# Performance work log

Measured on AMD Instinct MI355X. Metric: run time of the kernel, lower is better.

The kernel has to match this reference:

```python
import jax, jax.numpy as jnp
import numpy as np


def setup_inputs() -> dict:
    key = jax.random.key(0)
    k1, k2, k3, k4, k5 = jax.random.split(key, 5)
    B, N, E, C_in, C_out, K = 64, 4096, 16, 64, 64, 3
    return {
        "x": jax.random.normal(k1, (B, N, C_in), dtype=jnp.float32),
        "adj_matrix": jax.random.normal(k2, (N, E), dtype=jnp.float32),
        "adj_embeddings": jax.random.normal(k3, (E, N), dtype=jnp.float32),
        "weights": jax.random.normal(k4, (K, C_in, C_out), dtype=jnp.float32) * 0.1,
        "bias": jax.random.normal(k5, (C_out,), dtype=jnp.float32) * 0.1,
    }


def reference(x, adj_matrix, adj_embeddings, weights, bias):
    # x: [B, N, C_in]; adj_matrix: [N, E]; adj_embeddings: [E, N]
    N = adj_matrix.shape[0]
    cheb_k = weights.shape[0]
    # adaptive adjacency: softmax(relu(adj @ emb), axis=1) -> [N, N]
    supports = jax.nn.softmax(jax.nn.relu(adj_matrix @ adj_embeddings), axis=1)
    # Chebyshev polynomial recursion: T0 = I, T1 = supports,
    # Tk = 2*supports @ T_{k-1} - T_{k-2}
    support_set = [jnp.eye(N, dtype=supports.dtype), supports]
    for _ in range(2, cheb_k):
        support_set.append(2.0 * supports @ support_set[-1] - support_set[-2])
    supports_k = jnp.stack(support_set, axis=0)  # [K, N, N]
    # aggregate: [K,N,M] x [B,M,C] -> [B,N,K,C]
    x_g = jnp.einsum("knm,bmc->bnkc", supports_k, x)
    # mix: [B,N,K,Cin] x [K,Cin,Cout] -> [B,N,Cout]
    return jnp.einsum("bnki,kio->bno", x_g, weights) + bias
```

## Files before the change

### kernel.cpp

```cpp
#include <hip/hip_runtime.h>


typedef __bf16 bf16;
typedef __bf16 bf16x8 __attribute__((ext_vector_type(8)));
typedef float f32x4 __attribute__((ext_vector_type(4)));

__device__ __forceinline__ void async_lds16(const void* g, void* l) {
  __builtin_amdgcn_global_load_lds((const __attribute__((address_space(1))) void*)g,
                                   (__attribute__((address_space(3))) void*)l, 16, 0, 0);
}

#define FENCE() asm volatile("" ::: "memory")
#define BAR()                          \
  do {                                 \
    FENCE();                           \
    __builtin_amdgcn_s_barrier();      \
    FENCE();                           \
  } while (0)
#define WAIT_VM(n) asm volatile("s_waitcnt vmcnt(" #n ")" ::: "memory")

__global__ __launch_bounds__(256) void build_wcat_k(const float* __restrict__ w, bf16* __restrict__ Wc) {
  int idx = blockIdx.x * 256 + threadIdx.x;
  if (idx >= 64 * 192) return;
  int o = idx / 192, kk = idx - o * 192;
  int k = kk >> 6, i = kk & 63;
  float v;
  if (k == 0)      v = w[i * 64 + o] - w[2 * 4096 + i * 64 + o];
  else if (k == 1) v = w[4096 + i * 64 + o];
  else             v = 2.f * w[2 * 4096 + i * 64 + o];
  Wc[idx] = (bf16)v;
}

__global__ __launch_bounds__(256) void supports_k(const float* __restrict__ adj,
                                                  const float* __restrict__ emb,
                                                  bf16* __restrict__ S) {
  __shared__ float sadj[8][16];
  __shared__ float sred[4];
  const int tid = threadIdx.x;
  const int n0 = blockIdx.x * 8;
  if (tid < 128) sadj[tid >> 4][tid & 15] = adj[n0 * 16 + tid];
  __syncthreads();
  for (int r = 0; r < 8; ++r) {
    float vals[16];
    float mx = 0.f;
    #pragma unroll
    for (int it = 0; it < 16; ++it) {
      const int j = it * 256 + tid;
      float v = 0.f;
      #pragma unroll
      for (int e = 0; e < 16; ++e) v = fmaf(sadj[r][e], emb[e * 4096 + j], v);
      v = fmaxf(v, 0.f);
      vals[it] = v;
      mx = fmaxf(mx, v);
    }
    #pragma unroll
    for (int off = 32; off > 0; off >>= 1) mx = fmaxf(mx, __shfl_xor(mx, off, 64));
    if ((tid & 63) == 0) sred[tid >> 6] = mx;
    __syncthreads();
    mx = fmaxf(fmaxf(sred[0], sred[1]), fmaxf(sred[2], sred[3]));
    float sum = 0.f;
    #pragma unroll
    for (int it = 0; it < 16; ++it) {
      float ev = __expf(vals[it] - mx);
      vals[it] = ev;
      sum += ev;
    }
    #pragma unroll
    for (int off = 32; off > 0; off >>= 1) sum += __shfl_xor(sum, off, 64);
    __syncthreads();
    if ((tid & 63) == 0) sred[tid >> 6] = sum;
    __syncthreads();
    const float inv = 1.f / (sred[0] + sred[1] + sred[2] + sred[3]);
    bf16* Srow = S + (n0 + r) * 4096;
    #pragma unroll
    for (int it = 0; it < 16; ++it) Srow[it * 256 + tid] = (bf16)(vals[it] * inv);
    __syncthreads();
  }
}

__global__ __launch_bounds__(256) void xpose_x_k(const float* __restrict__ x, bf16* __restrict__ Xt) {
  __shared__ float tile[64][65];
  const int tid = threadIdx.x;
  const int mt = blockIdx.x, b = blockIdx.y;
  const float* src = x + (b * 4096 + mt * 64) * 64;
  #pragma unroll
  for (int it = 0; it < 16; ++it) {
    const int idx = it * 256 + tid;
    tile[idx >> 6][idx & 63] = src[idx];
  }
  __syncthreads();
  #pragma unroll
  for (int it = 0; it < 16; ++it) {
    const int idx = it * 256 + tid;
    const int rr = idx >> 6, cc = idx & 63;
    Xt[(b * 64 + rr) * 4096 + mt * 64 + cc] = (bf16)tile[cc][rr];
  }
}

__global__ __launch_bounds__(256) void transpose_bf16_k(const bf16* __restrict__ in, bf16* __restrict__ outT) {
  __shared__ bf16 tile[64][65];
  const int tid = threadIdx.x;
  const int ti = blockIdx.x & 63, tj = blockIdx.x >> 6;
  #pragma unroll
  for (int it = 0; it < 16; ++it) {
    const int idx = it * 256 + tid;
    tile[idx >> 6][idx & 63] = in[(ti * 64 + (idx >> 6)) * 4096 + tj * 64 + (idx & 63)];
  }
  __syncthreads();
  #pragma unroll
  for (int it = 0; it < 16; ++it) {
    const int idx = it * 256 + tid;
    const int rr = idx >> 6, cc = idx & 63;
    outT[(tj * 64 + rr) * 4096 + ti * 64 + cc] = tile[cc][rr];
  }
}

__global__ __launch_bounds__(512, 2) void gemm256_k(const bf16* __restrict__ A,
                                                    const bf16* __restrict__ Bt,
                                                    bf16* __restrict__ C) {
  __shared__ bf16 As[2][2][256][32];
  __shared__ bf16 Bs[2][2][256][32];

  const int tid = threadIdx.x;
  const int bid = blockIdx.x;
  const int wg = (bid & 7) * 32 + (bid >> 3);
  const int tm = wg >> 4, tn = wg & 15;
  const int rowBase = tm * 256, colBase = tn * 256;

  const int wv = tid >> 6, lane = tid & 63;
  const int wm = wv >> 2, wn = wv & 3;
  const int t16 = lane & 15, quad = lane >> 4;
  const int wv16 = wv * 16;
  const int q8 = (quad ^ ((t16 >> 1) & 3)) * 8;
  const int wm128 = wm * 128;
  const int wn64 = wn * 64;

  const int sr = tid >> 2;
  const int sc = ((tid & 3) ^ ((tid >> 3) & 3)) * 8;
  const bf16* gA = A + (size_t)(rowBase + sr) * 4096 + sc;
  const bf16* gB = Bt + (size_t)(colBase + sr) * 4096 + sc;

  f32x4 acc[8][4];
  #pragma unroll
  for (int i = 0; i < 8; ++i)
    #pragma unroll
    for (int j = 0; j < 4; ++j) acc[i][j] = (f32x4){0.f, 0.f, 0.f, 0.f};

  auto stA = [&](int buf, int s, int k0) {
    async_lds16(gA + k0 + s * 32, &As[buf][s][wv16][0]);
    async_lds16(gA + 524288 + k0 + s * 32, &As[buf][s][128 + wv16][0]);
  };
  auto stB = [&](int buf, int s, int k0) {
    async_lds16(gB + k0 + s * 32, &Bs[buf][s][wv16][0]);
    async_lds16(gB + 524288 + k0 + s * 32, &Bs[buf][s][128 + wv16][0]);
  };

  bf16x8 Ra[4], Rb[4], B0[4], B1[4];
  auto rdA = [&](bf16x8* R, int buf, int s, int g) {
    #pragma unroll
    for (int i = 0; i < 4; ++i)
      R[i] = *(const bf16x8*)&As[buf][s][wm128 + (g * 4 + i) * 16 + t16][q8];
  };
  auto rdB = [&](bf16x8* R, int buf, int s) {
    #pragma unroll
    for (int j = 0; j < 4; ++j)
      R[j] = *(const bf16x8*)&Bs[buf][s][wn64 + j * 16 + t16][q8];
  };
  auto mfma16 = [&](int g, const bf16x8* R, const bf16x8* Bv) {
    __builtin_amdgcn_s_setprio(1);
    #pragma unroll
    for (int i = 0; i < 4; ++i)
      #pragma unroll
      for (int j = 0; j < 4; ++j)
        acc[g * 4 + i][j] =
            __builtin_amdgcn_mfma_f32_16x16x32_bf16(R[i], Bv[j], acc[g * 4 + i][j], 0, 0, 0);
    __builtin_amdgcn_s_setprio(0);
  };

  stB(0, 0, 0); stA(0, 0, 0); stB(0, 1, 0); stA(0, 1, 0);
  stB(1, 0, 64); stA(1, 0, 64); stB(1, 1, 64);
  WAIT_VM(6);
  BAR();
  rdA(Ra, 0, 0, 0);
  rdB(B0, 0, 0);

  for (int it = 0; it < 31; ++it) {
    const int kb = it * 128;
    rdA(Rb, 0, 0, 1); stA(1, 1, kb + 64);
    BAR(); mfma16(0, Ra, B0); BAR();
    rdA(Ra, 0, 1, 0); rdB(B1, 0, 1); stB(0, 0, kb + 128);
    BAR(); mfma16(1, Rb, B0); BAR();
    rdA(Rb, 0, 1, 1); stA(0, 0, kb + 128);
    BAR(); mfma16(0, Ra, B1); BAR();
    stB(0, 1, kb + 128); WAIT_VM(6);
    BAR();
    rdA(Ra, 1, 0, 0); rdB(B0, 1, 0);
    mfma16(1, Rb, B1); BAR();
    rdA(Rb, 1, 0, 1); stA(0, 1, kb + 128);
    BAR(); mfma16(0, Ra, B0); BAR();
    rdA(Ra, 1, 1, 0); rdB(B1, 1, 1); stB(1, 0, kb + 192);
    BAR(); mfma16(1, Rb, B0); BAR();
    rdA(Rb, 1, 1, 1); stA(1, 0, kb + 192);
    BAR(); mfma16(0, Ra, B1); BAR();
    stB(1, 1, kb + 192); WAIT_VM(6);
    BAR();
    rdA(Ra, 0, 0, 0); rdB(B0, 0, 0);
    mfma16(1, Rb, B1); BAR();
  }

  rdA(Rb, 0, 0, 1); stA(1, 1, 4032);
  BAR(); mfma16(0, Ra, B0); BAR();
  rdA(Ra, 0, 1, 0); rdB(B1, 0, 1);
  BAR(); mfma16(1, Rb, B0); BAR();
  rdA(Rb, 0, 1, 1);
  BAR(); mfma16(0, Ra, B1); BAR();
  WAIT_VM(0);
  BAR();
  rdA(Ra, 1, 0, 0); rdB(B0, 1, 0);
  mfma16(1, Rb, B1); BAR();
  rdA(Rb, 1, 0, 1);
  mfma16(0, Ra, B0);
  rdA(Ra, 1, 1, 0); rdB(B1, 1, 1);
  mfma16(1, Rb, B0);
  rdA(Rb, 1, 1, 1);
  mfma16(0, Ra, B1);
  mfma16(1, Rb, B1);

  #pragma unroll
  for (int i = 0; i < 8; ++i) {
    const int row0 = rowBase + wm128 + i * 16 + quad * 4;
    #pragma unroll
    for (int j = 0; j < 4; ++j) {
      const int col = colBase + wn64 + j * 16 + t16;
      #pragma unroll
      for (int rr = 0; rr < 4; ++rr)
        C[(size_t)(row0 + rr) * 4096 + col] = (bf16)acc[i][j][rr];
    }
  }
}

__global__ __launch_bounds__(256) void mix_k(const float* __restrict__ x, const bf16* __restrict__ XG1,
                                             const bf16* __restrict__ XG2, const bf16* __restrict__ Wc,
                                             const float* __restrict__ bias, float* __restrict__ out) {
  __shared__ bf16 sW[64 * 200];
  const int tid = threadIdx.x;
  const int nt = blockIdx.x, b = blockIdx.y;
  {
    const int rw = tid >> 2, part = tid & 3;
    #pragma unroll
    for (int v = 0; v < 6; ++v)
      *(bf16x8*)(sW + rw * 200 + part * 48 + v * 8) = *(const bf16x8*)(Wc + rw * 192 + part * 48 + v * 8);
  }
  __syncthreads();

  const int lane = tid & 63, wv = tid >> 6;
  const int t16 = lane & 15, quad = lane >> 4;
  const int nBase = nt * 128 + wv * 32;

  f32x4 acc[2][4];
  #pragma unroll
  for (int i = 0; i < 2; ++i)
    #pragma unroll
    for (int j = 0; j < 4; ++j) acc[i][j] = (f32x4){0.f, 0.f, 0.f, 0.f};

  #pragma unroll
  for (int ch = 0; ch < 6; ++ch) {
    bf16x8 a[2];
    #pragma unroll
    for (int i = 0; i < 2; ++i) {
      const int row = nBase + i * 16 + t16;
      if (ch < 2) {
        const float* p = x + (b * 4096 + row) * 64 + ch * 32 + quad * 8;
        float4 f0 = *(const float4*)p;
        float4 f1 = *(const float4*)(p + 4);
        bf16x8 t;
        t[0] = (bf16)f0.x; t[1] = (bf16)f0.y; t[2] = (bf16)f0.z; t[3] = (bf16)f0.w;
        t[4] = (bf16)f1.x; t[5] = (bf16)f1.y; t[6] = (bf16)f1.z; t[7] = (bf16)f1.w;
        a[i] = t;
      } else {
        const bf16* src = (ch < 4) ? XG1 : XG2;
        a[i] = *(const bf16x8*)(src + row * 4096 + b * 64 + (ch & 1) * 32 + quad * 8);
      }
    }
    #pragma unroll
    for (int j = 0; j < 4; ++j) {
      bf16x8 wf = *(const bf16x8*)(sW + (j * 16 + t16) * 200 + ch * 32 + quad * 8);
      #pragma unroll
      for (int i = 0; i < 2; ++i)
        acc[i][j] = __builtin_amdgcn_mfma_f32_16x16x32_bf16(a[i], wf, acc[i][j], 0, 0, 0);
    }
  }

  #pragma unroll
  for (int j = 0; j < 4; ++j) {
    const float bb = bias[j * 16 + t16];
    #pragma unroll
    for (int i = 0; i < 2; ++i) {
      const int n0 = nBase + i * 16 + quad * 4;
      #pragma unroll
      for (int rr = 0; rr < 4; ++rr)
        out[(b * 4096 + n0 + rr) * 64 + j * 16 + t16] = acc[i][j][rr] + bb;
    }
  }
}

extern "C" void kernel_launch(void* const* d_in, const int* in_sizes, int n_in,
                              void* d_out, int out_size, void* d_ws, size_t ws_size,
                              hipStream_t stream) {
  const float* x    = (const float*)d_in[0];
  const float* adj  = (const float*)d_in[1];
  const float* emb  = (const float*)d_in[2];
  const float* w    = (const float*)d_in[3];
  const float* bias = (const float*)d_in[4];
  float* out = (float*)d_out;

  char* ws = (char*)d_ws;
  const size_t SZ = (size_t)4096 * 4096 * sizeof(bf16);
  bf16* S    = (bf16*)(ws);
  bf16* XG1  = (bf16*)(ws + SZ);
  bf16* XG2  = (bf16*)(ws + 2 * SZ);
  bf16* XBUF = (bf16*)(ws + 3 * SZ);
  bf16* Wc   = (bf16*)(ws + 4 * SZ);

  build_wcat_k<<<48, 256, 0, stream>>>(w, Wc);
  supports_k<<<512, 256, 0, stream>>>(adj, emb, S);
  xpose_x_k<<<dim3(64, 64), 256, 0, stream>>>(x, XBUF);
  gemm256_k<<<256, 512, 0, stream>>>(S, XBUF, XG1);
  transpose_bf16_k<<<4096, 256, 0, stream>>>(XG1, XBUF);
  gemm256_k<<<256, 512, 0, stream>>>(S, XBUF, XG2);
  mix_k<<<dim3(32, 64), 256, 0, stream>>>(x, XG1, XG2, Wc, bias, out);
}
```

Baseline: 445.0 us.

## Restructure GEMM barrier schedule and fuse transposed store of first GEMM output

The GEMM main loop is reordered so each LDS read group is followed directly by its MFMA block with a single barrier per phase, where before every MFMA block was bracketed by two barriers. The aim is less barrier overhead and more overlap of LDS reads with matrix math. Separately, the first GEMM now also writes its output transposed into an extra workspace buffer, so the standalone transpose kernel is skipped when the workspace is large enough. This costs extra strided 8-byte global stores in the epilogue and one more buffer of workspace.

```diff
diff --git a/kernel.cpp b/kernel.cpp
--- a/kernel.cpp
+++ b/kernel.cpp
@@ -117,7 +117,8 @@
 
 __global__ __launch_bounds__(512, 2) void gemm256_k(const bf16* __restrict__ A,
                                                     const bf16* __restrict__ Bt,
-                                                    bf16* __restrict__ C) {
+                                                    bf16* __restrict__ C,
+                                                    bf16* __restrict__ Ct) {
   __shared__ bf16 As[2][2][256][32];
   __shared__ bf16 Bs[2][2][256][32];
 
@@ -181,44 +182,57 @@
   stB(1, 0, 64); stA(1, 0, 64); stB(1, 1, 64);
   WAIT_VM(6);
   BAR();
-  rdA(Ra, 0, 0, 0);
-  rdB(B0, 0, 0);
 
   for (int it = 0; it < 31; ++it) {
     const int kb = it * 128;
-    rdA(Rb, 0, 0, 1); stA(1, 1, kb + 64);
-    BAR(); mfma16(0, Ra, B0); BAR();
-    rdA(Ra, 0, 1, 0); rdB(B1, 0, 1); stB(0, 0, kb + 128);
-    BAR(); mfma16(1, Rb, B0); BAR();
-    rdA(Rb, 0, 1, 1); stA(0, 0, kb + 128);
-    BAR(); mfma16(0, Ra, B1); BAR();
-    stB(0, 1, kb + 128); WAIT_VM(6);
-    BAR();
-    rdA(Ra, 1, 0, 0); rdB(B0, 1, 0);
-    mfma16(1, Rb, B1); BAR();
-    rdA(Rb, 1, 0, 1); stA(0, 1, kb + 128);
-    BAR(); mfma16(0, Ra, B0); BAR();
-    rdA(Ra, 1, 1, 0); rdB(B1, 1, 1); stB(1, 0, kb + 192);
-    BAR(); mfma16(1, Rb, B0); BAR();
-    rdA(Rb, 1, 1, 1); stA(1, 0, kb + 192);
-    BAR(); mfma16(0, Ra, B1); BAR();
-    stB(1, 1, kb + 192); WAIT_VM(6);
-    BAR();
-    rdA(Ra, 0, 0, 0); rdB(B0, 0, 0);
-    mfma16(1, Rb, B1); BAR();
-  }
-
-  rdA(Rb, 0, 0, 1); stA(1, 1, 4032);
-  BAR(); mfma16(0, Ra, B0); BAR();
+    rdA(Ra, 0, 0, 0); rdB(B0, 0, 0); rdA(Rb, 0, 0, 1);
+    stA(1, 1, kb + 64);
+    mfma16(0, Ra, B0);
+    BAR();
+    rdA(Ra, 0, 1, 0); rdB(B1, 0, 1);
+    stB(0, 0, kb + 128);
+    mfma16(1, Rb, B0);
+    BAR();
+    rdA(Rb, 0, 1, 1);
+    stA(0, 0, kb + 128);
+    mfma16(0, Ra, B1);
+    BAR();
+    stB(0, 1, kb + 128);
+    mfma16(1, Rb, B1);
+    WAIT_VM(6);
+    BAR();
+    rdA(Ra, 1, 0, 0); rdB(B0, 1, 0); rdA(Rb, 1, 0, 1);
+    stA(0, 1, kb + 128);
+    mfma16(0, Ra, B0);
+    BAR();
+    rdA(Ra, 1, 1, 0); rdB(B1, 1, 1);
+    stB(1, 0, kb + 192);
+    mfma16(1, Rb, B0);
+    BAR();
+    rdA(Rb, 1, 1, 1);
+    stA(1, 0, kb + 192);
+    mfma16(0, Ra, B1);
+    BAR();
+    stB(1, 1, kb + 192);
+    mfma16(1, Rb, B1);
+    WAIT_VM(6);
+    BAR();
+  }
+
+  rdA(Ra, 0, 0, 0); rdB(B0, 0, 0); rdA(Rb, 0, 0, 1);
+  stA(1, 1, 4032);
+  mfma16(0, Ra, B0);
+  BAR();
   rdA(Ra, 0, 1, 0); rdB(B1, 0, 1);
-  BAR(); mfma16(1, Rb, B0); BAR();
+  mfma16(1, Rb, B0);
+  BAR();
   rdA(Rb, 0, 1, 1);
-  BAR(); mfma16(0, Ra, B1); BAR();
+  mfma16(0, Ra, B1);
+  BAR();
+  mfma16(1, Rb, B1);
   WAIT_VM(0);
   BAR();
-  rdA(Ra, 1, 0, 0); rdB(B0, 1, 0);
-  mfma16(1, Rb, B1); BAR();
-  rdA(Rb, 1, 0, 1);
+  rdA(Ra, 1, 0, 0); rdB(B0, 1, 0); rdA(Rb, 1, 0, 1);
   mfma16(0, Ra, B0);
   rdA(Ra, 1, 1, 0); rdB(B1, 1, 1);
   mfma16(1, Rb, B0);
@@ -235,6 +249,20 @@
       #pragma unroll
       for (int rr = 0; rr < 4; ++rr)
         C[(size_t)(row0 + rr) * 4096 + col] = (bf16)acc[i][j][rr];
+    }
+  }
+  if (Ct) {
+    #pragma unroll
+    for (int i = 0; i < 8; ++i) {
+      const int row0 = rowBase + wm128 + i * 16 + quad * 4;
+      #pragma unroll
+      for (int j = 0; j < 4; ++j) {
+        const int col = colBase + wn64 + j * 16 + t16;
+        union { bf16 h[4]; uint2 u; } pk;
+        #pragma unroll
+        for (int rr = 0; rr < 4; ++rr) pk.h[rr] = (bf16)acc[i][j][rr];
+        *(uint2*)(Ct + (size_t)col * 4096 + row0) = pk.u;
+      }
     }
   }
 }
@@ -320,13 +348,15 @@
   bf16* XG1  = (bf16*)(ws + SZ);
   bf16* XG2  = (bf16*)(ws + 2 * SZ);
   bf16* XBUF = (bf16*)(ws + 3 * SZ);
-  bf16* Wc   = (bf16*)(ws + 4 * SZ);
+  const bool fused_t = ws_size >= 5 * SZ + (size_t)(64 * 192 * sizeof(bf16));
+  bf16* XG1T = fused_t ? (bf16*)(ws + 4 * SZ) : XBUF;
+  bf16* Wc   = (bf16*)(ws + (fused_t ? 5 : 4) * SZ);
 
   build_wcat_k<<<48, 256, 0, stream>>>(w, Wc);
   supports_k<<<512, 256, 0, stream>>>(adj, emb, S);
   xpose_x_k<<<dim3(64, 64), 256, 0, stream>>>(x, XBUF);
-  gemm256_k<<<256, 512, 0, stream>>>(S, XBUF, XG1);
-  transpose_bf16_k<<<4096, 256, 0, stream>>>(XG1, XBUF);
-  gemm256_k<<<256, 512, 0, stream>>>(S, XBUF, XG2);
+  gemm256_k<<<256, 512, 0, stream>>>(S, XBUF, XG1, fused_t ? XG1T : nullptr);
+  if (!fused_t) transpose_bf16_k<<<4096, 256, 0, stream>>>(XG1, XBUF);
+  gemm256_k<<<256, 512, 0, stream>>>(S, XG1T, XG2, nullptr);
   mix_k<<<dim3(32, 64), 256, 0, stream>>>(x, XG1, XG2, Wc, bias, out);
 }
```

Result: faster. 434.1 us (-2.4%).
